# Performance work log

Hardware: AMD Instinct MI355X
Metric: run time of the kernel (lower is better)

## Reference

```python
import jax, jax.numpy as jnp
import numpy as np

B, N, L = 64, 256, 1024
OUT = L // 2   # ChebConv out_channels = Seq_len / 2
ALPHA = 0.5    # DirGNNConv default alpha


def _glorot(key, shape):
    # PyG ChebConv lins use glorot init
    lim = float(np.sqrt(6.0 / (shape[0] + shape[1])))
    return jax.random.uniform(key, shape, minval=-lim, maxval=lim, dtype=jnp.float32)


def setup_inputs() -> dict:
    key = jax.random.key(0)
    ks = jax.random.split(key, 8)
    x = jax.random.normal(ks[0], (B, N, L), dtype=jnp.float32)
    # dense per-sample adjacency; only used via nonzero() in torch, never enters math (K=1)
    At = jax.random.randint(ks[1], (B, N, N), 0, 2, dtype=jnp.int32)
    W_in = _glorot(ks[2], (L, OUT))
    b_in = jnp.zeros((OUT,), dtype=jnp.float32)
    W_out = _glorot(ks[3], (L, OUT))
    b_out = jnp.zeros((OUT,), dtype=jnp.float32)
    # DirGNNConv root Linear (kaiming-ish uniform; exact init irrelevant for correctness baseline)
    lim = float(1.0 / np.sqrt(L))
    W_root = jax.random.uniform(ks[4], (L, OUT), minval=-lim, maxval=lim, dtype=jnp.float32)
    b_root = jax.random.uniform(ks[5], (OUT,), minval=-lim, maxval=lim, dtype=jnp.float32)
    return {"x": x, "At": At, "W_in": W_in, "b_in": b_in,
            "W_out": W_out, "b_out": b_out, "W_root": W_root, "b_root": b_root}


def reference(x, At, W_in, b_in, W_out, b_out, W_root, b_root):
    # so the batched edge_index built from At.nonzero() never influences the output.
    # DirGNNConv: alpha * conv_out(x) + (1-alpha) * conv_in(x) + root_lin(x).
    xf = x.reshape(B * N, L)                        # [B*N, L]
    y = (ALPHA * (xf @ W_out + b_out)
         + (1.0 - ALPHA) * (xf @ W_in + b_in)
         + (xf @ W_root + b_root))                  # [B*N, OUT]
    return y.reshape(B, N, OUT)
```

## Files before the change

kernel.cpp:

```cpp
#include <hip/hip_runtime.h>
#include <stdint.h>

static constexpr int Kdim  = 1024;
static constexpr int Ncols = 512;

typedef __attribute__((ext_vector_type(8))) short bf16x8;
typedef __attribute__((ext_vector_type(4))) float f32x4;

union pk8 { uint4 u; bf16x8 h; };

__device__ __forceinline__ unsigned short f2bf(float f) {
  unsigned u = __builtin_bit_cast(unsigned, f);
  u += 0x7FFFu + ((u >> 16) & 1u);
  return (unsigned short)(u >> 16);
}
__device__ __forceinline__ unsigned f2bf2(float lo, float hi) {
  unsigned ul = __builtin_bit_cast(unsigned, lo);
  unsigned uh = __builtin_bit_cast(unsigned, hi);
  ul += 0x7FFFu + ((ul >> 16) & 1u);
  uh += 0x7FFFu + ((uh >> 16) & 1u);
  return (ul >> 16) | (uh & 0xFFFF0000u);
}

__device__ __forceinline__ void gl2lds16(const void* g, void* l) {
  __builtin_amdgcn_global_load_lds(
      (const __attribute__((address_space(1))) void*)g,
      (__attribute__((address_space(3))) void*)l, 16, 0, 0);
}

__global__ __launch_bounds__(256) void combine_w(
    const float* __restrict__ Win, const float* __restrict__ Wout,
    const float* __restrict__ Wroot, unsigned short* __restrict__ Wt)
{
  __shared__ unsigned short lds[32 * 36];
  const int bid = blockIdx.x;
  const int tk0 = (bid & 31) * 32;
  const int tn0 = (bid >> 5) * 32;
  const int t = threadIdx.x;
  {
    const int k  = t >> 3;
    const int nq = (t & 7) * 4;
    const int gi = (tk0 + k) * Ncols + tn0 + nq;
    const float4 wi = *(const float4*)(Win + gi);
    const float4 wo = *(const float4*)(Wout + gi);
    const float4 wr = *(const float4*)(Wroot + gi);
    lds[(nq + 0) * 36 + k] = f2bf(0.5f * (wi.x + wo.x) + wr.x);
    lds[(nq + 1) * 36 + k] = f2bf(0.5f * (wi.y + wo.y) + wr.y);
    lds[(nq + 2) * 36 + k] = f2bf(0.5f * (wi.z + wo.z) + wr.z);
    lds[(nq + 3) * 36 + k] = f2bf(0.5f * (wi.w + wo.w) + wr.w);
  }
  __syncthreads();
  {
    const int n  = t >> 3;
    const int k8 = (t & 7) * 4;
    const ushort4 v = *(const ushort4*)&lds[n * 36 + k8];
    *(ushort4*)(Wt + (size_t)(tn0 + n) * Kdim + tk0 + k8) = v;
  }
}

__global__ __launch_bounds__(512, 2) void gemm_fullN(
    const float* __restrict__ X, const unsigned short* __restrict__ Wt,
    const float* __restrict__ b_in, const float* __restrict__ b_out,
    const float* __restrict__ b_root, float* __restrict__ Y)
{
  __shared__ __attribute__((aligned(16))) float As[2][64 * 32];
  __shared__ __attribute__((aligned(16))) short Bs[2][512 * 32];

  const int m0 = blockIdx.x * 64;

  const int t    = threadIdx.x;
  const int lane = t & 63;
  const int w    = t >> 6;
  const int quad = lane >> 4;
  const int lm   = lane & 15;

  const int ra = lane >> 3;
  const int ca = (lane & 7) ^ ra;
  const float* gA = X + (size_t)(m0 + w * 8 + ra) * Kdim + ca * 4;
  float* const lA = &As[0][0] + (w * 8) * 32;
  const int bufA = 64 * 32;

  const int rb = lane >> 2;
  const int cb = (lane & 3) ^ ((rb >> 1) & 3);
  const unsigned short* gB = Wt + (size_t)(w * 64 + rb) * Kdim + cb * 8;
  short* const lB = &Bs[0][0] + (w * 64) * 32;
  const int bufB = 512 * 32;
  const int rowK16 = 16 * Kdim;

  const int sA0   = (2 * quad) ^ (lm & 7);
  const int slotB = quad ^ ((lm >> 1) & 3);
  const int aoff  = lm * 32;
  const int boff  = (w * 64 + lm) * 32 + slotB * 8;

  f32x4 acc[4][4] = {};

  gl2lds16(gA, lA);
  #pragma unroll
  for (int g = 0; g < 4; ++g)
    gl2lds16(gB + (size_t)g * rowK16, lB + g * 512);

  #pragma unroll 1
  for (int it = 0; it < 32; ++it) {
    const int p = (it & 1);
    const int q = p ^ 1;
    __syncthreads();

    if (it != 31) {
      const int nx = (it + 1) * 32;
      gl2lds16(gA + nx, lA + q * bufA);
      #pragma unroll
      for (int g = 0; g < 4; ++g)
        gl2lds16(gB + nx + (size_t)g * rowK16, lB + q * bufB + g * 512);
    }

    const float* Ap = &As[0][0] + p * bufA;
    const short* Bp = &Bs[0][0] + p * bufB;

    bf16x8 bfr[4];
    #pragma unroll
    for (int j = 0; j < 4; ++j)
      bfr[j] = *(const bf16x8*)&Bp[boff + j * 512];

    bf16x8 af[4];
    #pragma unroll
    for (int i = 0; i < 4; ++i) {
      const f32x4 lo = *(const f32x4*)&Ap[i * 512 + aoff + sA0 * 4];
      const f32x4 hi = *(const f32x4*)&Ap[i * 512 + aoff + (sA0 ^ 1) * 4];
      pk8 pk;
      pk.u.x = f2bf2(lo.x, lo.y);
      pk.u.y = f2bf2(lo.z, lo.w);
      pk.u.z = f2bf2(hi.x, hi.y);
      pk.u.w = f2bf2(hi.z, hi.w);
      af[i] = pk.h;
    }

    #pragma unroll
    for (int i = 0; i < 4; ++i)
      #pragma unroll
      for (int j = 0; j < 4; ++j)
        acc[i][j] = __builtin_amdgcn_mfma_f32_16x16x32_bf16(af[i], bfr[j], acc[i][j], 0, 0, 0);
  }

  #pragma unroll
  for (int j = 0; j < 4; ++j) {
    const int gc = w * 64 + j * 16 + lm;
    const float bias = 0.5f * (b_in[gc] + b_out[gc]) + b_root[gc];
    #pragma unroll
    for (int i = 0; i < 4; ++i) {
      const int gr = m0 + i * 16 + quad * 4;
      float* yp = Y + (size_t)gr * Ncols + gc;
      #pragma unroll
      for (int r = 0; r < 4; ++r)
        yp[(size_t)r * Ncols] = acc[i][j][r] + bias;
    }
  }
}

extern "C" void kernel_launch(void* const* d_in, const int* in_sizes, int n_in,
                              void* d_out, int out_size, void* d_ws, size_t ws_size,
                              hipStream_t stream)
{
  const float* x      = (const float*)d_in[0];
  const float* W_in   = (const float*)d_in[2];
  const float* b_in   = (const float*)d_in[3];
  const float* W_out  = (const float*)d_in[4];
  const float* b_out  = (const float*)d_in[5];
  const float* W_root = (const float*)d_in[6];
  const float* b_root = (const float*)d_in[7];
  float* y = (float*)d_out;

  unsigned short* Wt = (unsigned short*)d_ws;

  combine_w <<<dim3(512), dim3(256), 0, stream>>>(W_in, W_out, W_root, Wt);
  gemm_fullN<<<dim3(256), dim3(512), 0, stream>>>(x, Wt, b_in, b_out, b_root, y);
}
```

Baseline: 165.7 us.

## Retile GEMM to 128x128 blocks with BK=64 and 32x32 MFMA

```diff
diff --git a/kernel.cpp b/kernel.cpp
--- a/kernel.cpp
+++ b/kernel.cpp
@@ -4,10 +4,8 @@
 static constexpr int Kdim  = 1024;
 static constexpr int Ncols = 512;
 
-typedef __attribute__((ext_vector_type(8))) short bf16x8;
-typedef __attribute__((ext_vector_type(4))) float f32x4;
-
-union pk8 { uint4 u; bf16x8 h; };
+typedef __attribute__((ext_vector_type(8)))  short bf16x8;
+typedef __attribute__((ext_vector_type(16))) float f32x16;
 
 __device__ __forceinline__ unsigned short f2bf(float f) {
   unsigned u = __builtin_bit_cast(unsigned, f);
@@ -58,100 +56,101 @@
   }
 }
 
-__global__ __launch_bounds__(512, 2) void gemm_fullN(
+__global__ __launch_bounds__(256, 2) void gemm_bk64(
     const float* __restrict__ X, const unsigned short* __restrict__ Wt,
     const float* __restrict__ b_in, const float* __restrict__ b_out,
     const float* __restrict__ b_root, float* __restrict__ Y)
 {
-  __shared__ __attribute__((aligned(16))) float As[2][64 * 32];
-  __shared__ __attribute__((aligned(16))) short Bs[2][512 * 32];
+  __shared__ __attribute__((aligned(16))) short As[128 * 64];
+  __shared__ __attribute__((aligned(16))) short Bs[128 * 64];
 
-  const int m0 = blockIdx.x * 64;
+  const int bid = blockIdx.x;
+  const int m0 = (bid & 127) * 128;
+  const int n0 = (bid >> 7) * 128;
 
   const int t    = threadIdx.x;
   const int lane = t & 63;
   const int w    = t >> 6;
-  const int quad = lane >> 4;
-  const int lm   = lane & 15;
+  const int wm   = w >> 1;
+  const int wn   = w & 1;
+  const int l31  = lane & 31;
+  const int khalf = lane >> 5;
 
-  const int ra = lane >> 3;
-  const int ca = (lane & 7) ^ ra;
-  const float* gA = X + (size_t)(m0 + w * 8 + ra) * Kdim + ca * 4;
-  float* const lA = &As[0][0] + (w * 8) * 32;
-  const int bufA = 64 * 32;
+  const int r  = t >> 1;
+  const int h  = t & 1;
+  const float* xp = X + (size_t)(m0 + r) * Kdim + h * 32;
+  const int rsw = r & 7;
+  int awr[4];
+  #pragma unroll
+  for (int c = 0; c < 4; ++c) awr[c] = r * 64 + (((h * 4 + c) ^ rsw) * 8);
 
-  const int rb = lane >> 2;
-  const int cb = (lane & 3) ^ ((rb >> 1) & 3);
-  const unsigned short* gB = Wt + (size_t)(w * 64 + rb) * Kdim + cb * 8;
-  short* const lB = &Bs[0][0] + (w * 64) * 32;
-  const int bufB = 512 * 32;
-  const int rowK16 = 16 * Kdim;
+  const int rb = lane >> 3;
+  const int sb = lane & 7;
+  const int cb = sb ^ (rb & 7);
+  const unsigned short* gB = Wt + (size_t)(n0 + w * 32 + rb) * Kdim + cb * 8;
+  short* const lB = &Bs[(w * 32) * 64];
+  const int rowK8 = 8 * Kdim;
 
-  const int sA0   = (2 * quad) ^ (lm & 7);
-  const int slotB = quad ^ ((lm >> 1) & 3);
-  const int aoff  = lm * 32;
-  const int boff  = (w * 64 + lm) * 32 + slotB * 8;
+  const int fsw = l31 & 7;
+  const int arow0 = (wm * 64 + l31) * 64;
+  const int brow0 = (wn * 64 + l31) * 64;
 
-  f32x4 acc[4][4] = {};
-
-  gl2lds16(gA, lA);
-  #pragma unroll
-  for (int g = 0; g < 4; ++g)
-    gl2lds16(gB + (size_t)g * rowK16, lB + g * 512);
+  f32x16 acc[2][2] = {};
 
   #pragma unroll 1
-  for (int it = 0; it < 32; ++it) {
-    const int p = (it & 1);
-    const int q = p ^ 1;
+  for (int it = 0; it < 16; ++it) {
+    const int kb = it * 64;
+
+    #pragma unroll
+    for (int g = 0; g < 4; ++g)
+      gl2lds16(gB + kb + (size_t)g * rowK8, lB + g * 8 * 64);
+
+    const float* xi = xp + kb;
+    float4 v[8];
+    #pragma unroll
+    for (int c = 0; c < 8; ++c) v[c] = *(const float4*)(xi + c * 4);
+    #pragma unroll
+    for (int c = 0; c < 4; ++c) {
+      uint4 pk;
+      pk.x = f2bf2(v[2 * c].x,     v[2 * c].y);
+      pk.y = f2bf2(v[2 * c].z,     v[2 * c].w);
+      pk.z = f2bf2(v[2 * c + 1].x, v[2 * c + 1].y);
+      pk.w = f2bf2(v[2 * c + 1].z, v[2 * c + 1].w);
+      *(uint4*)&As[awr[c]] = pk;
+    }
+
     __syncthreads();
 
-    if (it != 31) {
-      const int nx = (it + 1) * 32;
-      gl2lds16(gA + nx, lA + q * bufA);
-      #pragma unroll
-      for (int g = 0; g < 4; ++g)
-        gl2lds16(gB + nx + (size_t)g * rowK16, lB + q * bufB + g * 512);
+    #pragma unroll
+    for (int ks = 0; ks < 4; ++ks) {
+      const int slot = ((ks * 2 + khalf) ^ fsw) * 8;
+      bf16x8 a0 = *(const bf16x8*)&As[arow0 +           slot];
+      bf16x8 a1 = *(const bf16x8*)&As[arow0 + 32 * 64 + slot];
+      bf16x8 b0 = *(const bf16x8*)&Bs[brow0 +           slot];
+      bf16x8 b1 = *(const bf16x8*)&Bs[brow0 + 32 * 64 + slot];
+      acc[0][0] = __builtin_amdgcn_mfma_f32_32x32x16_bf16(a0, b0, acc[0][0], 0, 0, 0);
+      acc[0][1] = __builtin_amdgcn_mfma_f32_32x32x16_bf16(a0, b1, acc[0][1], 0, 0, 0);
+      acc[1][0] = __builtin_amdgcn_mfma_f32_32x32x16_bf16(a1, b0, acc[1][0], 0, 0, 0);
+      acc[1][1] = __builtin_amdgcn_mfma_f32_32x32x16_bf16(a1, b1, acc[1][1], 0, 0, 0);
     }
 
-    const float* Ap = &As[0][0] + p * bufA;
-    const short* Bp = &Bs[0][0] + p * bufB;
-
-    bf16x8 bfr[4];
-    #pragma unroll
-    for (int j = 0; j < 4; ++j)
-      bfr[j] = *(const bf16x8*)&Bp[boff + j * 512];
-
-    bf16x8 af[4];
-    #pragma unroll
-    for (int i = 0; i < 4; ++i) {
-      const f32x4 lo = *(const f32x4*)&Ap[i * 512 + aoff + sA0 * 4];
-      const f32x4 hi = *(const f32x4*)&Ap[i * 512 + aoff + (sA0 ^ 1) * 4];
-      pk8 pk;
-      pk.u.x = f2bf2(lo.x, lo.y);
-      pk.u.y = f2bf2(lo.z, lo.w);
-      pk.u.z = f2bf2(hi.x, hi.y);
-      pk.u.w = f2bf2(hi.z, hi.w);
-      af[i] = pk.h;
-    }
-
-    #pragma unroll
-    for (int i = 0; i < 4; ++i)
-      #pragma unroll
-      for (int j = 0; j < 4; ++j)
-        acc[i][j] = __builtin_amdgcn_mfma_f32_16x16x32_bf16(af[i], bfr[j], acc[i][j], 0, 0, 0);
+    __syncthreads();
   }
 
   #pragma unroll
-  for (int j = 0; j < 4; ++j) {
-    const int gc = w * 64 + j * 16 + lm;
+  for (int nj = 0; nj < 2; ++nj) {
+    const int gc = n0 + wn * 64 + nj * 32 + l31;
     const float bias = 0.5f * (b_in[gc] + b_out[gc]) + b_root[gc];
     #pragma unroll
-    for (int i = 0; i < 4; ++i) {
-      const int gr = m0 + i * 16 + quad * 4;
-      float* yp = Y + (size_t)gr * Ncols + gc;
+    for (int mi = 0; mi < 2; ++mi) {
+      const int gr0 = m0 + wm * 64 + mi * 32 + 4 * khalf;
       #pragma unroll
-      for (int r = 0; r < 4; ++r)
-        yp[(size_t)r * Ncols] = acc[i][j][r] + bias;
+      for (int g = 0; g < 4; ++g) {
+        float* yp = Y + (size_t)(gr0 + 8 * g) * Ncols + gc;
+        #pragma unroll
+        for (int q = 0; q < 4; ++q)
+          yp[(size_t)q * Ncols] = acc[mi][nj][4 * g + q] + bias;
+      }
     }
   }
 }
@@ -171,6 +170,6 @@
 
   unsigned short* Wt = (unsigned short*)d_ws;
 
-  combine_w <<<dim3(512), dim3(256), 0, stream>>>(W_in, W_out, W_root, Wt);
-  gemm_fullN<<<dim3(256), dim3(512), 0, stream>>>(x, Wt, b_in, b_out, b_root, y);
+  combine_w<<<dim3(512), dim3(256), 0, stream>>>(W_in, W_out, W_root, Wt);
+  gemm_bk64<<<dim3(512), dim3(256), 0, stream>>>(x, Wt, b_in, b_out, b_root, y);
 }
```

Measured after the change: 170.4 us. 2.8% more time.
